# Kernel optimization log

Hardware: AMD Instinct MI355X
Metric: run time of the kernel (lower is better)

## Reference

```python
import jax, jax.numpy as jnp
import numpy as np

N = 20000      # nodes
E = 320000     # edges (avg degree 16)
D = 128        # emb_dim
L = 5          # num_layer
NV = 119       # node vocab (atom types)
EV = 5         # edge vocab (bond types)
BN_EPS = 1e-5


def setup_inputs() -> dict:
    key = jax.random.key(0)
    ks = jax.random.split(key, 8)
    s = 0.1
    return {
        "x": jax.random.randint(ks[0], (N,), 0, NV),
        "edge_index": jax.random.randint(ks[1], (2, E), 0, N),
        "edge_attr": jax.random.randint(ks[2], (E,), 0, EV),
        "node_emb1": jax.random.normal(ks[3], (NV, D), jnp.float32) * s,
        "node_emb2": jax.random.normal(ks[4], (NV, D), jnp.float32) * s,
        "edge_emb": jax.random.normal(ks[5], (2, L, EV, D), jnp.float32) * s,
        "eps": jnp.zeros((2, L), jnp.float32),
        "W": jax.random.normal(ks[6], (2, L, D, D), jnp.float32) / np.sqrt(D).astype(np.float32),
        "b": jnp.zeros((2, L, D), jnp.float32),
        "bn_gamma": jnp.ones((2, L, D), jnp.float32),
        "bn_beta": jnp.zeros((2, L, D), jnp.float32),
        "cross_unit": jnp.full((L, 2, 2), 0.5, jnp.float32),
    }


def gin_conv(h, src, dst, eattr, edge_tab, eps, W, b):
    # message: relu(x_j + edge_embedding), aggregated by add at target nodes
    msg = jax.nn.relu(h[src] + edge_tab[eattr])            # [E, D]
    agg = jax.ops.segment_sum(msg, dst, num_segments=h.shape[0])  # [N, D]
    return ((1.0 + eps) * h + agg) @ W.T + b               # mlp = single Linear


def batch_norm(h, gamma, beta):
    # training-mode BatchNorm1d over the node dimension (biased variance)
    mu = h.mean(axis=0)
    var = h.var(axis=0)
    return (h - mu) * jax.lax.rsqrt(var + BN_EPS) * gamma + beta


def reference(x, edge_index, edge_attr, node_emb1, node_emb2, edge_emb, eps, W, b,
              bn_gamma, bn_beta, cross_unit):
    src, dst = edge_index[0], edge_index[1]
    h1 = node_emb1[x]   # NodeEncoder tower 1
    h2 = node_emb2[x]   # NodeEncoder tower 2
    for l in range(L):
        a1 = gin_conv(h1, src, dst, edge_attr, edge_emb[0, l], eps[0, l], W[0, l], b[0, l])
        a1 = batch_norm(a1, bn_gamma[0, l], bn_beta[0, l])
        a2 = gin_conv(h2, src, dst, edge_attr, edge_emb[1, l], eps[1, l], W[1, l], b[1, l])
        a2 = batch_norm(a2, bn_gamma[1, l], bn_beta[1, l])
        if l < L - 1:
            a1 = jax.nn.relu(a1)
            a2 = jax.nn.relu(a2)
        # dropout: identity (eval mode / deterministic reference)
        # cross-stitch; note h_2 uses the UPDATED h_1 (faithful to source)
        c = cross_unit[l]
        n1 = c[0, 0] * a1 + c[0, 1] * a2
        n2 = c[1, 0] * n1 + c[1, 1] * a2
        h1, h2 = n1, n2
    return (h1, h2)  # JK == 'last'
```

## Files before the change

### kernel.cpp

```cpp
#include <hip/hip_runtime.h>

#define NN 20000
#define EE 320000
#define DD 128
#define LL 5
#define EVV 5
#define BNEPS 1e-5f
#define FB 1250
#define EMB_BLOCKS 2500
#define CVT_BLOCKS 160
#define CNT_BLOCKS 1250

typedef __attribute__((ext_vector_type(8))) short bf8_t;
typedef __attribute__((ext_vector_type(4))) float f4_t;
typedef __attribute__((ext_vector_type(8))) unsigned short us8;

__device__ inline unsigned short f2bf(float f) {
    union { float f; unsigned u; } v;
    v.f = f;
    unsigned r = v.u + 0x7fffu + ((v.u >> 16) & 1u);
    return (unsigned short)(r >> 16);
}
__device__ inline float bf2f(unsigned short h) {
    union { unsigned u; float f; } v;
    v.u = ((unsigned)h) << 16;
    return v.f;
}
__device__ inline float4 bf2f4(ushort4 u) {
    float4 f;
    f.x = bf2f(u.x); f.y = bf2f(u.y); f.z = bf2f(u.z); f.w = bf2f(u.w);
    return f;
}
__device__ inline float4 add4(float4 a, float4 b) {
    float4 r;
    r.x = a.x + b.x; r.y = a.y + b.y; r.z = a.z + b.z; r.w = a.w + b.w;
    return r;
}

__device__ inline void xform4(float4 v1, float4 v2,
                              float4 s1, float4 t1, float4 s2, float4 t2,
                              float c00, float c01, float c10, float c11,
                              int dorelu, float4& n1, float4& n2) {
    float x1, x2, m1, m2;
#define XE(f)                                                    \
    x1 = v1.f * s1.f + t1.f;                                     \
    x2 = v2.f * s2.f + t2.f;                                     \
    x1 = dorelu ? fmaxf(x1, 0.f) : x1;                           \
    x2 = dorelu ? fmaxf(x2, 0.f) : x2;                           \
    m1 = c00 * x1 + c01 * x2;                                    \
    m2 = c10 * m1 + c11 * x2;                                    \
    n1.f = m1;                                                   \
    n2.f = m2;
    XE(x) XE(y) XE(z) XE(w)
#undef XE
}

__device__ inline void bn_coeffs(const float* __restrict__ statsL,
                                 const float* __restrict__ gall,
                                 const float* __restrict__ btall,
                                 int pl, int c,
                                 float4& s1, float4& t1, float4& s2, float4& t2) {
    const float inv = 1.0f / (float)NN;
    int ch = c * 4;
#define BNC(tw, sv, tv)                                                       \
    {                                                                         \
        const float* gp = gall + (size_t)((tw) * LL + pl) * DD + ch;          \
        const float* bp = btall + (size_t)((tw) * LL + pl) * DD + ch;         \
        float r[4];                                                           \
        _Pragma("unroll") for (int j = 0; j < 4; j++) {                       \
            float sum = statsL[(tw) * 256 + ch + j];                          \
            float sq = statsL[(tw) * 256 + 128 + ch + j];                     \
            float mu = sum * inv;                                             \
            float var = sq * inv - mu * mu;                                   \
            float rs = rsqrtf(var + BNEPS);                                   \
            float sc = rs * gp[j];                                            \
            r[j] = sc;                                                        \
            ((float*)&tv)[j] = bp[j] - mu * sc;                               \
        }                                                                     \
        sv.x = r[0]; sv.y = r[1]; sv.z = r[2]; sv.w = r[3];                   \
    }
    BNC(0, s1, t1)
    BNC(1, s2, t2)
#undef BNC
}

__device__ inline ushort4 hi4(float4 v) {
    ushort4 h;
    h.x = f2bf(v.x); h.y = f2bf(v.y); h.z = f2bf(v.z); h.w = f2bf(v.w);
    return h;
}
__device__ inline ushort4 lo4(float4 v, ushort4 h) {
    ushort4 l;
    l.x = f2bf(v.x - bf2f(h.x)); l.y = f2bf(v.y - bf2f(h.y));
    l.z = f2bf(v.z - bf2f(h.z)); l.w = f2bf(v.w - bf2f(h.w));
    return l;
}


__global__ __launch_bounds__(256) void prep_kernel(
    const int* __restrict__ x,
    const float4* __restrict__ e1, const float4* __restrict__ e2,
    ushort4* __restrict__ eh, ushort4* __restrict__ el,
    const float4* __restrict__ Wall,
    ushort4* __restrict__ Wbh, ushort4* __restrict__ Wbl,
    const int* __restrict__ dst, int* __restrict__ deg,
    float* __restrict__ stats,
    const float* __restrict__ etab, unsigned short* __restrict__ etb2) {
    int bid = blockIdx.x;
    int tid = threadIdx.x;
    if (bid < EMB_BLOCKS) {
        int idx = bid * 256 + tid;
        int r = idx >> 5, c = idx & 31;
        int v = x[r];
        float4 w1 = e1[v * 32 + c];
        float4 w2 = e2[v * 32 + c];
        ushort4 h = hi4(w1);
        eh[(size_t)r * 64 + c] = h;
        el[(size_t)r * 64 + c] = lo4(w1, h);
        h = hi4(w2);
        eh[(size_t)r * 64 + 32 + c] = h;
        el[(size_t)r * 64 + 32 + c] = lo4(w2, h);
    } else if (bid < EMB_BLOCKS + CVT_BLOCKS) {
        int i = (bid - EMB_BLOCKS) * 256 + tid;
        float4 w = Wall[i];
        ushort4 oh = hi4(w);
        Wbh[i] = oh;
        Wbl[i] = lo4(w, oh);
    } else if (bid < EMB_BLOCKS + CVT_BLOCKS + CNT_BLOCKS) {
        int e = (bid - EMB_BLOCKS - CVT_BLOCKS) * 256 + tid;
        atomicAdd(&deg[dst[e]], 1);
    } else {
#pragma unroll
        for (int i = 0; i < 10; i++) stats[i * 256 + tid] = 0.f;
        for (int idx = tid; idx < 2 * LL * EVV * DD; idx += 256) {
            int ch = idx & 127;
            int tw = (idx >> 7) & 1;
            int la = idx >> 8;
            int a = la % EVV;
            int l = la / EVV;
            etb2[idx] = f2bf(etab[((size_t)(tw * LL + l) * EVV + a) * DD + ch]);
        }
    }
}


__global__ __launch_bounds__(1024) void scan_kernel(const int* __restrict__ deg,
                                                    int* __restrict__ offs,
                                                    int* __restrict__ pos) {
    __shared__ int wsum[16];
    int t = threadIdx.x;
    int lane = t & 63, wv = t >> 6;
    int base = t * 20;
    int loc[20];
    int s = 0;
#pragma unroll
    for (int i = 0; i < 20; i++) {
        int j = base + i;
        int d = (j < NN) ? deg[j] : 0;
        loc[i] = d;
        s += d;
    }
    int incl = s;
#pragma unroll
    for (int o = 1; o < 64; o <<= 1) {
        int v = __shfl_up(incl, o, 64);
        if (lane >= o) incl += v;
    }
    if (lane == 63) wsum[wv] = incl;
    __syncthreads();
    if (t < 16) {
        int v = wsum[t];
        int iv = v;
#pragma unroll
        for (int o = 1; o < 16; o <<= 1) {
            int u = __shfl_up(iv, o, 64);
            if (t >= o) iv += u;
        }
        wsum[t] = iv - v;
    }
    __syncthreads();
    int run = wsum[wv] + (incl - s);
#pragma unroll
    for (int i = 0; i < 20; i++) {
        int j = base + i;
        if (j < NN) {
            offs[j] = run;
            pos[j] = run;
            run += loc[i];
        }
    }
}

__global__ __launch_bounds__(256) void scatter_kernel(const int* __restrict__ src,
                                                      const int* __restrict__ dst,
                                                      const int* __restrict__ eattr,
                                                      int* __restrict__ pos,
                                                      int2* __restrict__ erec) {
    int e = blockIdx.x * 256 + threadIdx.x;
    if (e < EE) {
        int d = dst[e];
        int p = atomicAdd(&pos[d], 1);
        erec[p] = make_int2(src[e], eattr[e]);
    }
}


__global__ __launch_bounds__(256) void xform_kernel(
    const ushort4* __restrict__ yh, const ushort4* __restrict__ yl,
    ushort4* __restrict__ hph, ushort4* __restrict__ hpl,
    const float* __restrict__ statsL,
    const float* __restrict__ gall, const float* __restrict__ btall,
    const float* __restrict__ crossp, int pl) {
    int idx = blockIdx.x * 256 + threadIdx.x;
    int r = idx >> 5, c = idx & 31;
    float4 s1, t1, s2, t2;
    bn_coeffs(statsL, gall, btall, pl, c, s1, t1, s2, t2);
    float c00 = crossp[0], c01 = crossp[1], c10 = crossp[2], c11 = crossp[3];
    float4 v1 = add4(bf2f4(yh[(size_t)r * 64 + c]), bf2f4(yl[(size_t)r * 64 + c]));
    float4 v2 = add4(bf2f4(yh[(size_t)r * 64 + 32 + c]), bf2f4(yl[(size_t)r * 64 + 32 + c]));
    float4 n1, n2;
    xform4(v1, v2, s1, t1, s2, t2, c00, c01, c10, c11, 1, n1, n2);
    ushort4 h = hi4(n1);
    hph[(size_t)r * 64 + c] = h;
    hpl[(size_t)r * 64 + c] = lo4(n1, h);
    h = hi4(n2);
    hph[(size_t)r * 64 + 32 + c] = h;
    hpl[(size_t)r * 64 + 32 + c] = lo4(n2, h);
}


__global__ __launch_bounds__(1024, 8) void agg_gemm_kernel(
    const us8* __restrict__ hph, const us8* __restrict__ hpl,
    const us8* __restrict__ etb2, int layer,
    const int* __restrict__ offs, const int* __restrict__ deg,
    const int2* __restrict__ erec, const float* __restrict__ epsall,
    const unsigned short* __restrict__ Wbh, const unsigned short* __restrict__ Wbl,
    const float* __restrict__ ball,
    unsigned short* __restrict__ yh, unsigned short* __restrict__ yl,
    float* __restrict__ statsL) {
    __shared__ float accS[16 * 8 * 33];
    __shared__ float sP[2][2][DD];
    us8* uS = (us8*)accS;

    int tid = threadIdx.x;
    int w = tid >> 6, lane = tid & 63;

    {
        int row = w;
        int node = blockIdx.x * 16 + row;
        int slot = lane >> 5;
        int c = lane & 31;
        const us8* et = etb2 + (size_t)layer * EVV * 32;
        float ep = 1.0f + epsall[(c >> 4) * LL + layer];

        int off = offs[node];
        int dg = deg[node];
        float a[8];
#pragma unroll
        for (int k = 0; k < 8; k++) a[k] = 0.f;
        int i = 0;
        for (; i + 8 <= dg; i += 8) {
            int2 r0 = erec[off + i + slot];
            int2 r1 = erec[off + i + 2 + slot];
            int2 r2 = erec[off + i + 4 + slot];
            int2 r3 = erec[off + i + 6 + slot];
            us8 h0 = hph[(size_t)r0.x * 32 + c];
            us8 h1 = hph[(size_t)r1.x * 32 + c];
            us8 h2 = hph[(size_t)r2.x * 32 + c];
            us8 h3 = hph[(size_t)r3.x * 32 + c];
            us8 e0 = et[r0.y * 32 + c];
            us8 e1 = et[r1.y * 32 + c];
            us8 e2 = et[r2.y * 32 + c];
            us8 e3 = et[r3.y * 32 + c];
#pragma unroll
            for (int k = 0; k < 8; k++) {
                a[k] += fmaxf(bf2f(h0[k]) + bf2f(e0[k]), 0.f);
                a[k] += fmaxf(bf2f(h1[k]) + bf2f(e1[k]), 0.f);
                a[k] += fmaxf(bf2f(h2[k]) + bf2f(e2[k]), 0.f);
                a[k] += fmaxf(bf2f(h3[k]) + bf2f(e3[k]), 0.f);
            }
        }
        for (; i < dg; i += 2) {
            int j = i + slot;
            bool valid = j < dg;
            int e = off + (valid ? j : 0);
            int2 r = erec[e];
            us8 h = hph[(size_t)r.x * 32 + c];
            us8 ev = et[r.y * 32 + c];
            if (valid) {
#pragma unroll
                for (int k = 0; k < 8; k++) a[k] += fmaxf(bf2f(h[k]) + bf2f(ev[k]), 0.f);
            }
        }
#pragma unroll
        for (int k = 0; k < 8; k++) a[k] += __shfl_xor(a[k], 32, 64);

        us8 sh = hph[(size_t)node * 32 + c];
        us8 sl = hpl[(size_t)node * 32 + c];
        us8 uh, ul;
#pragma unroll
        for (int k = 0; k < 8; k++) {
            float u = ep * (bf2f(sh[k]) + bf2f(sl[k])) + a[k];
            unsigned short h = f2bf(u);
            uh[k] = h;
            ul[k] = f2bf(u - bf2f(h));
        }
        int unit = slot * 32 + c;
        uS[row * 64 + (unit ^ (row & 7))] = slot ? ul : uh;
    }
    __syncthreads();

    int tw = w >> 3, nt = w & 7;
    int quad = lane >> 4, m = lane & 15;
    const bf8_t* Wh8 = (const bf8_t*)(Wbh + (size_t)(tw * LL + layer) * DD * DD);
    const bf8_t* Wl8 = (const bf8_t*)(Wbl + (size_t)(tw * LL + layer) * DD * DD);
    const float* bias = ball + (size_t)(tw * LL + layer) * DD;
    const bf8_t* u8 = (const bf8_t*)uS;

    f4_t acc;
    acc[0] = 0.f; acc[1] = 0.f; acc[2] = 0.f; acc[3] = 0.f;
    int lrow = m;
    int sw = lrow & 7;
#pragma unroll
    for (int kt = 0; kt < 4; kt++) {
        int x = kt * 4 + quad;
        bf8_t ah = u8[lrow * 64 + (tw * 16 + (x ^ sw))];
        bf8_t al = u8[lrow * 64 + (32 + tw * 16 + (x ^ sw))];
        bf8_t bh = Wh8[(nt * 16 + m) * 16 + x];
        bf8_t bl = Wl8[(nt * 16 + m) * 16 + x];
        acc = __builtin_amdgcn_mfma_f32_16x16x32_bf16(ah, bh, acc, 0, 0, 0);
        acc = __builtin_amdgcn_mfma_f32_16x16x32_bf16(al, bh, acc, 0, 0, 0);
        acc = __builtin_amdgcn_mfma_f32_16x16x32_bf16(ah, bl, acc, 0, 0, 0);
    }
    __syncthreads();

    {
        int col = nt * 16 + m;
        float bv = bias[col];
        int gc = tw * 128 + col;
        int cg = gc >> 5, kk = gc & 31;
        float s = 0.f, q = 0.f;
#pragma unroll
        for (int r = 0; r < 4; r++) {
            int lr2 = quad * 4 + r;
            float v = acc[r] + bv;
            accS[(lr2 * 8 + cg) * 33 + kk] = v;
            s += v; q += v * v;
        }
        s += __shfl_xor(s, 16, 64); s += __shfl_xor(s, 32, 64);
        q += __shfl_xor(q, 16, 64); q += __shfl_xor(q, 32, 64);
        if (quad == 0) {
            sP[tw][0][col] = s;
            sP[tw][1][col] = q;
        }
    }
    __syncthreads();

    {
        int t = tid & 511;
        int row = t >> 5, unit = t & 31;
        int grow = blockIdx.x * 16 + row;
        int cg = unit >> 2, kb = (unit & 3) * 8;
        const float* srcp = accS + (row * 8 + cg) * 33 + kb;
        us8 v8;
        if (tid < 512) {
#pragma unroll
            for (int k = 0; k < 8; k++) v8[k] = f2bf(srcp[k]);
            ((us8*)yh)[(size_t)grow * 32 + unit] = v8;
        } else {
#pragma unroll
            for (int k = 0; k < 8; k++) {
                float v = srcp[k];
                v8[k] = f2bf(v - bf2f(f2bf(v)));
            }
            ((us8*)yl)[(size_t)grow * 32 + unit] = v8;
        }
    }

    if (tid < 512) {
        int twi = tid >> 8, idx = tid & 255;
        int sq = idx >> 7, ch = idx & 127;
        atomicAdd(&statsL[twi * 256 + idx], sP[twi][sq][ch]);
    }
}


__global__ __launch_bounds__(256) void bn_final_kernel(
    const ushort4* __restrict__ yh, const ushort4* __restrict__ yl,
    float4* __restrict__ o1, float4* __restrict__ o2,
    const float* __restrict__ statsL,
    const float* __restrict__ gall, const float* __restrict__ btall,
    const float* __restrict__ crossp) {
    int idx = blockIdx.x * 256 + threadIdx.x;
    int r = idx >> 5, c = idx & 31;
    float4 s1, t1, s2, t2;
    bn_coeffs(statsL, gall, btall, LL - 1, c, s1, t1, s2, t2);
    float c00 = crossp[0], c01 = crossp[1], c10 = crossp[2], c11 = crossp[3];
    float4 v1 = add4(bf2f4(yh[(size_t)r * 64 + c]), bf2f4(yl[(size_t)r * 64 + c]));
    float4 v2 = add4(bf2f4(yh[(size_t)r * 64 + 32 + c]), bf2f4(yl[(size_t)r * 64 + 32 + c]));
    float4 n1, n2;
    xform4(v1, v2, s1, t1, s2, t2, c00, c01, c10, c11, 0, n1, n2);
    o1[(size_t)r * 32 + c] = n1;
    o2[(size_t)r * 32 + c] = n2;
}


extern "C" void kernel_launch(void* const* d_in, const int* in_sizes, int n_in,
                              void* d_out, int out_size, void* d_ws, size_t ws_size,
                              hipStream_t stream) {
    const int* x = (const int*)d_in[0];
    const int* eidx = (const int*)d_in[1];
    const int* eattr = (const int*)d_in[2];
    const float* emb1 = (const float*)d_in[3];
    const float* emb2 = (const float*)d_in[4];
    const float* etab = (const float*)d_in[5];
    const float* epsv = (const float*)d_in[6];
    const float* Wall = (const float*)d_in[7];
    const float* ball = (const float*)d_in[8];
    const float* gall = (const float*)d_in[9];
    const float* btall = (const float*)d_in[10];
    const float* cross = (const float*)d_in[11];
    float* out = (float*)d_out;

    const size_t ND = (size_t)NN * DD;
    char* p = (char*)d_ws;
    unsigned short* yh = (unsigned short*)p;   p += (size_t)NN * 256 * 2;
    unsigned short* yl = (unsigned short*)p;   p += (size_t)NN * 256 * 2;
    unsigned short* hph = (unsigned short*)p;  p += (size_t)NN * 256 * 2;
    unsigned short* hpl = (unsigned short*)p;  p += (size_t)NN * 256 * 2;
    unsigned short* eh = (unsigned short*)p;   p += (size_t)NN * 256 * 2;
    unsigned short* el = (unsigned short*)p;   p += (size_t)NN * 256 * 2;
    unsigned short* Wbh = (unsigned short*)p;  p += (size_t)2 * LL * DD * DD * 2;
    unsigned short* Wbl = (unsigned short*)p;  p += (size_t)2 * LL * DD * DD * 2;
    unsigned short* etb2 = (unsigned short*)p; p += (size_t)2 * LL * EVV * DD * 2;
    int* deg = (int*)p;               p += (size_t)NN * 4;
    int* offs = (int*)p;              p += (size_t)NN * 4;
    int* pos = (int*)p;               p += (size_t)NN * 4;
    int2* erec = (int2*)p;            p += (size_t)EE * 8;
    float* stats = (float*)p;         p += (size_t)LL * 512 * 4;

    const int* src = eidx;
    const int* dst = eidx + EE;

    hipMemsetAsync(deg, 0, (size_t)NN * 4, stream);
    prep_kernel<<<EMB_BLOCKS + CVT_BLOCKS + CNT_BLOCKS + 1, 256, 0, stream>>>(
        x, (const float4*)emb1, (const float4*)emb2,
        (ushort4*)eh, (ushort4*)el,
        (const float4*)Wall, (ushort4*)Wbh, (ushort4*)Wbl, dst, deg, stats,
        etab, etb2);
    scan_kernel<<<1, 1024, 0, stream>>>(deg, offs, pos);
    scatter_kernel<<<EE / 256, 256, 0, stream>>>(src, dst, eattr, pos, erec);

    for (int l = 0; l < LL; l++) {
        const unsigned short* hsrc_h = eh;
        const unsigned short* hsrc_l = el;
        if (l > 0) {
            xform_kernel<<<(NN * 32) / 256, 256, 0, stream>>>(
                (const ushort4*)yh, (const ushort4*)yl,
                (ushort4*)hph, (ushort4*)hpl,
                stats + (size_t)(l - 1) * 512, gall, btall,
                cross + (l - 1) * 4, l - 1);
            hsrc_h = hph;
            hsrc_l = hpl;
        }
        agg_gemm_kernel<<<FB, 1024, 0, stream>>>(
            (const us8*)hsrc_h, (const us8*)hsrc_l, (const us8*)etb2, l,
            offs, deg, erec, epsv, Wbh, Wbl, ball, yh, yl,
            stats + (size_t)l * 512);
    }
    bn_final_kernel<<<(NN * 32) / 256, 256, 0, stream>>>(
        (const ushort4*)yh, (const ushort4*)yl, (float4*)out, (float4*)(out + ND),
        stats + (size_t)(LL - 1) * 512, gall, btall, cross + (LL - 1) * 4);
}
```

Before: 471.6 us.

## Fuse BN+relu+cross-stitch transform into aggregation gather, drop xform kernel

Removes the separate per-layer xform kernel and instead applies batch-norm affine, relu and the cross-stitch mix on the fly to each gathered neighbor row inside agg_gemm. The two towers are paired via a lane shuffle. Output buffers are ping-ponged so the previous layer's raw output can be read while the new one is written. This saves a full read/write pass over node features and a launch per layer, at the cost of redundant per-edge ALU work and shuffles in the gather loop.

```diff
diff --git a/kernel.cpp b/kernel.cpp
--- a/kernel.cpp
+++ b/kernel.cpp
@@ -94,6 +94,22 @@
     l.x = f2bf(v.x - bf2f(h.x)); l.y = f2bf(v.y - bf2f(h.y));
     l.z = f2bf(v.z - bf2f(h.z)); l.w = f2bf(v.w - bf2f(h.w));
     return l;
+}
+
+__device__ inline float foldv(float y, float s, float t,
+                              float c00, float c01, float c10, float c11,
+                              int isT1, int dorelu) {
+    float x = y * s + t;
+    x = dorelu ? fmaxf(x, 0.f) : x;
+    float p = __shfl_xor(x, 16, 64);
+    float n;
+    if (!isT1) {
+        n = c00 * x + c01 * p;
+    } else {
+        float n1 = c00 * p + c01 * x;
+        n = c10 * n1 + c11 * x;
+    }
+    return n;
 }
 
 
@@ -205,39 +221,18 @@
 }
 
 
-__global__ __launch_bounds__(256) void xform_kernel(
-    const ushort4* __restrict__ yh, const ushort4* __restrict__ yl,
-    ushort4* __restrict__ hph, ushort4* __restrict__ hpl,
-    const float* __restrict__ statsL,
-    const float* __restrict__ gall, const float* __restrict__ btall,
-    const float* __restrict__ crossp, int pl) {
-    int idx = blockIdx.x * 256 + threadIdx.x;
-    int r = idx >> 5, c = idx & 31;
-    float4 s1, t1, s2, t2;
-    bn_coeffs(statsL, gall, btall, pl, c, s1, t1, s2, t2);
-    float c00 = crossp[0], c01 = crossp[1], c10 = crossp[2], c11 = crossp[3];
-    float4 v1 = add4(bf2f4(yh[(size_t)r * 64 + c]), bf2f4(yl[(size_t)r * 64 + c]));
-    float4 v2 = add4(bf2f4(yh[(size_t)r * 64 + 32 + c]), bf2f4(yl[(size_t)r * 64 + 32 + c]));
-    float4 n1, n2;
-    xform4(v1, v2, s1, t1, s2, t2, c00, c01, c10, c11, 1, n1, n2);
-    ushort4 h = hi4(n1);
-    hph[(size_t)r * 64 + c] = h;
-    hpl[(size_t)r * 64 + c] = lo4(n1, h);
-    h = hi4(n2);
-    hph[(size_t)r * 64 + 32 + c] = h;
-    hpl[(size_t)r * 64 + 32 + c] = lo4(n2, h);
-}
-
-
 __global__ __launch_bounds__(1024, 8) void agg_gemm_kernel(
-    const us8* __restrict__ hph, const us8* __restrict__ hpl,
+    const us8* __restrict__ srcYh, const us8* __restrict__ srcYl,
     const us8* __restrict__ etb2, int layer,
     const int* __restrict__ offs, const int* __restrict__ deg,
     const int2* __restrict__ erec, const float* __restrict__ epsall,
     const unsigned short* __restrict__ Wbh, const unsigned short* __restrict__ Wbl,
     const float* __restrict__ ball,
     unsigned short* __restrict__ yh, unsigned short* __restrict__ yl,
-    float* __restrict__ statsL) {
+    float* __restrict__ statsL,
+    const float* __restrict__ statsPrev,
+    const float* __restrict__ gall, const float* __restrict__ btall,
+    const float* __restrict__ crossp) {
     __shared__ float accS[16 * 8 * 33];
     __shared__ float sP[2][2][DD];
     us8* uS = (us8*)accS;
@@ -250,8 +245,36 @@
         int node = blockIdx.x * 16 + row;
         int slot = lane >> 5;
         int c = lane & 31;
+        int isT1 = c >> 4;
         const us8* et = etb2 + (size_t)layer * EVV * 32;
-        float ep = 1.0f + epsall[(c >> 4) * LL + layer];
+        float ep = 1.0f + epsall[isT1 * LL + layer];
+
+        float sC[8], tC[8], c00, c01, c10, c11;
+        int dorelu;
+        if (layer == 0) {
+#pragma unroll
+            for (int k = 0; k < 8; k++) { sC[k] = 1.f; tC[k] = 0.f; }
+            c00 = 1.f; c01 = 0.f; c10 = 0.f; c11 = 1.f; dorelu = 0;
+        } else {
+            int ch0 = (c & 15) * 8;
+            const float inv = 1.0f / (float)NN;
+            const float* sp = statsPrev + isT1 * 256 + ch0;
+            const float* gp = gall + (size_t)(isT1 * LL + layer - 1) * DD + ch0;
+            const float* bp = btall + (size_t)(isT1 * LL + layer - 1) * DD + ch0;
+#pragma unroll
+            for (int k = 0; k < 8; k++) {
+                float sum = sp[k];
+                float sq = sp[128 + k];
+                float mu = sum * inv;
+                float var = sq * inv - mu * mu;
+                float rs = rsqrtf(var + BNEPS);
+                float sc = rs * gp[k];
+                sC[k] = sc;
+                tC[k] = bp[k] - mu * sc;
+            }
+            c00 = crossp[0]; c01 = crossp[1]; c10 = crossp[2]; c11 = crossp[3];
+            dorelu = 1;
+        }
 
         int off = offs[node];
         int dg = deg[node];
@@ -264,20 +287,24 @@
             int2 r1 = erec[off + i + 2 + slot];
             int2 r2 = erec[off + i + 4 + slot];
             int2 r3 = erec[off + i + 6 + slot];
-            us8 h0 = hph[(size_t)r0.x * 32 + c];
-            us8 h1 = hph[(size_t)r1.x * 32 + c];
-            us8 h2 = hph[(size_t)r2.x * 32 + c];
-            us8 h3 = hph[(size_t)r3.x * 32 + c];
+            us8 h0 = srcYh[(size_t)r0.x * 32 + c];
+            us8 h1 = srcYh[(size_t)r1.x * 32 + c];
+            us8 h2 = srcYh[(size_t)r2.x * 32 + c];
+            us8 h3 = srcYh[(size_t)r3.x * 32 + c];
             us8 e0 = et[r0.y * 32 + c];
             us8 e1 = et[r1.y * 32 + c];
             us8 e2 = et[r2.y * 32 + c];
             us8 e3 = et[r3.y * 32 + c];
 #pragma unroll
             for (int k = 0; k < 8; k++) {
-                a[k] += fmaxf(bf2f(h0[k]) + bf2f(e0[k]), 0.f);
-                a[k] += fmaxf(bf2f(h1[k]) + bf2f(e1[k]), 0.f);
-                a[k] += fmaxf(bf2f(h2[k]) + bf2f(e2[k]), 0.f);
-                a[k] += fmaxf(bf2f(h3[k]) + bf2f(e3[k]), 0.f);
+                float v0 = foldv(bf2f(h0[k]), sC[k], tC[k], c00, c01, c10, c11, isT1, dorelu);
+                float v1 = foldv(bf2f(h1[k]), sC[k], tC[k], c00, c01, c10, c11, isT1, dorelu);
+                float v2 = foldv(bf2f(h2[k]), sC[k], tC[k], c00, c01, c10, c11, isT1, dorelu);
+                float v3 = foldv(bf2f(h3[k]), sC[k], tC[k], c00, c01, c10, c11, isT1, dorelu);
+                a[k] += fmaxf(v0 + bf2f(e0[k]), 0.f);
+                a[k] += fmaxf(v1 + bf2f(e1[k]), 0.f);
+                a[k] += fmaxf(v2 + bf2f(e2[k]), 0.f);
+                a[k] += fmaxf(v3 + bf2f(e3[k]), 0.f);
             }
         }
         for (; i < dg; i += 2) {
@@ -285,22 +312,25 @@
             bool valid = j < dg;
             int e = off + (valid ? j : 0);
             int2 r = erec[e];
-            us8 h = hph[(size_t)r.x * 32 + c];
+            us8 h = srcYh[(size_t)r.x * 32 + c];
             us8 ev = et[r.y * 32 + c];
-            if (valid) {
-#pragma unroll
-                for (int k = 0; k < 8; k++) a[k] += fmaxf(bf2f(h[k]) + bf2f(ev[k]), 0.f);
+#pragma unroll
+            for (int k = 0; k < 8; k++) {
+                float v = foldv(bf2f(h[k]), sC[k], tC[k], c00, c01, c10, c11, isT1, dorelu);
+                if (valid) a[k] += fmaxf(v + bf2f(ev[k]), 0.f);
             }
         }
 #pragma unroll
         for (int k = 0; k < 8; k++) a[k] += __shfl_xor(a[k], 32, 64);
 
-        us8 sh = hph[(size_t)node * 32 + c];
-        us8 sl = hpl[(size_t)node * 32 + c];
+        us8 sh = srcYh[(size_t)node * 32 + c];
+        us8 sl = srcYl[(size_t)node * 32 + c];
         us8 uh, ul;
 #pragma unroll
         for (int k = 0; k < 8; k++) {
-            float u = ep * (bf2f(sh[k]) + bf2f(sl[k])) + a[k];
+            float v = bf2f(sh[k]) + bf2f(sl[k]);
+            float n = foldv(v, sC[k], tC[k], c00, c01, c10, c11, isT1, dorelu);
+            float u = ep * n + a[k];
             unsigned short h = f2bf(u);
             uh[k] = h;
             ul[k] = f2bf(u - bf2f(h));
@@ -424,10 +454,10 @@
 
     const size_t ND = (size_t)NN * DD;
     char* p = (char*)d_ws;
-    unsigned short* yh = (unsigned short*)p;   p += (size_t)NN * 256 * 2;
-    unsigned short* yl = (unsigned short*)p;   p += (size_t)NN * 256 * 2;
-    unsigned short* hph = (unsigned short*)p;  p += (size_t)NN * 256 * 2;
-    unsigned short* hpl = (unsigned short*)p;  p += (size_t)NN * 256 * 2;
+    unsigned short* yhA = (unsigned short*)p;  p += (size_t)NN * 256 * 2;
+    unsigned short* ylA = (unsigned short*)p;  p += (size_t)NN * 256 * 2;
+    unsigned short* yhB = (unsigned short*)p;  p += (size_t)NN * 256 * 2;
+    unsigned short* ylB = (unsigned short*)p;  p += (size_t)NN * 256 * 2;
     unsigned short* eh = (unsigned short*)p;   p += (size_t)NN * 256 * 2;
     unsigned short* el = (unsigned short*)p;   p += (size_t)NN * 256 * 2;
     unsigned short* Wbh = (unsigned short*)p;  p += (size_t)2 * LL * DD * DD * 2;
@@ -439,6 +469,9 @@
     int2* erec = (int2*)p;            p += (size_t)EE * 8;
     float* stats = (float*)p;         p += (size_t)LL * 512 * 4;
 
+    unsigned short* ybh[2] = { yhA, yhB };
+    unsigned short* ybl[2] = { ylA, ylB };
+
     const int* src = eidx;
     const int* dst = eidx + EE;
 
@@ -452,23 +485,18 @@
     scatter_kernel<<<EE / 256, 256, 0, stream>>>(src, dst, eattr, pos, erec);
 
     for (int l = 0; l < LL; l++) {
-        const unsigned short* hsrc_h = eh;
-        const unsigned short* hsrc_l = el;
-        if (l > 0) {
-            xform_kernel<<<(NN * 32) / 256, 256, 0, stream>>>(
-                (const ushort4*)yh, (const ushort4*)yl,
-                (ushort4*)hph, (ushort4*)hpl,
-                stats + (size_t)(l - 1) * 512, gall, btall,
-                cross + (l - 1) * 4, l - 1);
-            hsrc_h = hph;
-            hsrc_l = hpl;
-        }
+        const unsigned short* sH = (l == 0) ? eh : ybh[(l - 1) & 1];
+        const unsigned short* sL = (l == 0) ? el : ybl[(l - 1) & 1];
         agg_gemm_kernel<<<FB, 1024, 0, stream>>>(
-            (const us8*)hsrc_h, (const us8*)hsrc_l, (const us8*)etb2, l,
-            offs, deg, erec, epsv, Wbh, Wbl, ball, yh, yl,
-            stats + (size_t)l * 512);
+            (const us8*)sH, (const us8*)sL, (const us8*)etb2, l,
+            offs, deg, erec, epsv, Wbh, Wbl, ball,
+            ybh[l & 1], ybl[l & 1],
+            stats + (size_t)l * 512,
+            stats + (size_t)(l ? (l - 1) : 0) * 512,
+            gall, btall,
+            cross + (size_t)(l ? (l - 1) : 0) * 4);
     }
     bn_final_kernel<<<(NN * 32) / 256, 256, 0, stream>>>(
-        (const ushort4*)yh, (const ushort4*)yl, (float4*)out, (float4*)(out + ND),
+        (const ushort4*)yhA, (const ushort4*)ylA, (float4*)out, (float4*)(out + ND),
         stats + (size_t)(LL - 1) * 512, gall, btall, cross + (LL - 1) * 4);
 }
```

After: 688.1 us. 1.46x slower.
